# Kernel tuning notes

Hardware: AMD Instinct MI355X
Metric: run time of the kernel (lower is better)

Reference implementation:

```python
import jax, jax.numpy as jnp
import numpy as np

B, N, D, H = 128, 256, 256, 256
N_POWER_ITERS = 5  # matches spectral_norm(n_power_iterations=5)


def setup_inputs() -> dict:
    key = jax.random.key(0)
    ks = jax.random.split(key, 8)
    w = lambda k, shape: jax.random.normal(k, shape, dtype=jnp.float32) * 0.05
    return {
        "x": jax.random.normal(ks[0], (B, N, D), dtype=jnp.float32),
        "Wq": w(ks[1], (H, D)), "bq": w(ks[2], (H,)),
        "Wk": w(ks[3], (H, D)), "bk": w(ks[4], (H,)),
        "Wv": w(ks[5], (D, D)), "bv": w(ks[6], (D,)),
        "u0": jax.random.normal(ks[7], (D,), dtype=jnp.float32),
    }


def _l2norm(v, eps=1e-12):
    return v / (jnp.linalg.norm(v) + eps)


def _spectral_normalize(W, u0):
    # torch spectral_norm: power iteration (no grad) to get u, v; sigma = u^T W v (with grad)
    u = _l2norm(u0)
    v = _l2norm(W.T @ u)
    def body(i, uv):
        u, v = uv
        v = _l2norm(W.T @ u)
        u = _l2norm(W @ v)
        return (u, v)
    u, v = jax.lax.fori_loop(0, N_POWER_ITERS, body, (u, v))
    u = jax.lax.stop_gradient(u)
    v = jax.lax.stop_gradient(v)
    sigma = u @ (W @ v)
    return W / sigma


def reference(x, Wq, bq, Wk, bk, Wv, bv, u0):
    # torch Linear: y = x @ W.T + b, W is [out, in]
    q = jnp.einsum('bnd,hd->bnh', x, Wq) + bq          # [B, N, H]
    k = jnp.einsum('bnd,hd->bnh', x, Wk) + bk          # [B, N, H]
    Wv_sn = _spectral_normalize(Wv, u0)
    vals = jnp.einsum('bnd,od->bno', x, Wv_sn) + bv    # [B, N, D]
    scores = jnp.einsum('bnh,bmh->bnm', q, k)          # [B, N, N]
    # track_grads=False -> eigenvals detached; stop_gradient input so eig has no tangent path
    ev = jnp.linalg.eigvals(jax.lax.stop_gradient(scores))  # complex [B, N]
    rho = jnp.max(jnp.abs(ev), axis=-1)[:, None, None]      # spectral radius [B,1,1]
    attention = scores / rho
    weighted = jnp.einsum('bnm,bmd->bnd', attention, vals)  # [B, N, D]
    return weighted, attention
```

## Files before the change

kernel.cpp:

```cpp
#include <hip/hip_runtime.h>
#include <hip/hip_bf16.h>


#define NB 128
#define MAT 65536
#define BIG 8388608LL

typedef __attribute__((ext_vector_type(4))) float floatx4;
typedef __attribute__((ext_vector_type(4))) float f4v;
typedef __attribute__((ext_vector_type(8))) short short8v;
typedef __attribute__((ext_vector_type(4))) short short4v;

__device__ __forceinline__ short f2bf(float x) {
  union { float f; unsigned u; } v; v.f = x;
  unsigned r = v.u + 0x7fff + ((v.u >> 16) & 1);
  return (short)(r >> 16);
}
__device__ __forceinline__ float bf2f(short h) {
  union { unsigned u; float f; } v; v.u = ((unsigned)(unsigned short)h) << 16; return v.f;
}

template<bool TB, bool BATCHED>
__global__ __launch_bounds__(256) void gemm_mfma(
    const float* __restrict__ A, const float* __restrict__ B, float* __restrict__ C,
    long long sA, long long sB, long long sC,
    const float* __restrict__ bias,
    const float* __restrict__ scale_ptr, int sstride, int smode,
    float* __restrict__ norm_out,
    float* __restrict__ att_out,
    const float* __restrict__ B2, const float* __restrict__ bias2, float* __restrict__ C2,
    const float* __restrict__ B3, float* __restrict__ C3,
    const float* __restrict__ bsc, const float* __restrict__ bsb)
{
  __shared__ short sAhi[128 * 32], sAlo[128 * 32];
  __shared__ short sBhi[128 * 40], sBlo[128 * 40];

  int bz, m0, n0;
  if constexpr (BATCHED) {
    int lin = blockIdx.x;
    int xcd = lin & 7;
    int s = lin >> 3;
    bz = xcd * 16 + (s >> 2);
    int tile = s & 3;
    m0 = (tile >> 1) * 128;
    n0 = (tile & 1) * 128;
  } else {
    bz = 0;
    m0 = blockIdx.y * 128;
    n0 = (blockIdx.x & 1) * 128;
    int sel = blockIdx.x >> 1;
    if (sel == 1) { B = B2; bias = bias2; C = C2; }
    else if (sel == 2) { B = B3; bias = nullptr; C = C3; }
  }
  A += (long long)bz * sA;
  B += (long long)bz * sB;
  C += (long long)bz * sC;

  const int t = threadIdx.x;
  const int lane = t & 63;
  const int wave = t >> 6;
  const int wm = wave >> 1, wn = wave & 1;
  const int q = lane >> 4, c16 = lane & 15;

  float alpha = 1.0f;
  if (smode == 1) alpha = 1.0f / scale_ptr[bz * sstride];
  else if (smode == 2) alpha = scale_ptr[bz * sstride];

  float rinv_att = alpha;
  const bool do_att = (att_out != nullptr) && (n0 == 0);

  float binv = 1.0f;
  if (bsc) binv = 1.0f / bsc[0];

  floatx4 acc[4][4];
  #pragma unroll
  for (int i = 0; i < 4; i++)
    #pragma unroll
    for (int j = 0; j < 4; j++)
      acc[i][j] = (floatx4){0.f, 0.f, 0.f, 0.f};

  for (int k0 = 0; k0 < 256; k0 += 32) {
    #pragma unroll
    for (int i = 0; i < 4; i++) {
      int f = t + i * 256;
      int row = f >> 3, c4 = f & 7;
      f4v v = *(const f4v*)(A + (long long)(m0 + row) * 256 + k0 + c4 * 4);
      if (do_att)
        *(f4v*)(att_out + (long long)bz * MAT + (long long)(m0 + row) * 256 + k0 + c4 * 4)
            = v * rinv_att;
      short4v h, l;
      #pragma unroll
      for (int e = 0; e < 4; e++) {
        short hh = f2bf(v[e]);
        h[e] = hh;
        l[e] = f2bf(v[e] - bf2f(hh));
      }
      *(short4v*)&sAhi[row * 32 + c4 * 4] = h;
      *(short4v*)&sAlo[row * 32 + c4 * 4] = l;
    }
    if constexpr (TB) {
      #pragma unroll
      for (int i = 0; i < 4; i++) {
        int f = t + i * 256;
        int row = f >> 3, c4 = f & 7;
        f4v v = *(const f4v*)(B + (long long)(n0 + row) * 256 + k0 + c4 * 4);
        short4v h, l;
        #pragma unroll
        for (int e = 0; e < 4; e++) {
          short hh = f2bf(v[e]);
          h[e] = hh;
          l[e] = f2bf(v[e] - bf2f(hh));
        }
        *(short4v*)&sBhi[row * 40 + c4 * 4] = h;
        *(short4v*)&sBlo[row * 40 + c4 * 4] = l;
      }
      __syncthreads();
    } else {
      __shared__ float sT[32 * 132];
      #pragma unroll
      for (int i = 0; i < 4; i++) {
        int f = t + i * 256;
        int kk = f >> 5, n4 = f & 31;
        f4v v = *(const f4v*)(B + (long long)(k0 + kk) * 256 + n0 + n4 * 4);
        if (bsb) {
          #pragma unroll
          for (int e = 0; e < 4; e++) v[e] = v[e] * binv + bsb[n0 + n4 * 4 + e];
        }
        *(f4v*)&sT[kk * 132 + n4 * 4] = v;
      }
      __syncthreads();
      int n = t & 127, kh = t >> 7;
      short8v h0, h1, l0, l1;
      #pragma unroll
      for (int j = 0; j < 8; j++) {
        float x0 = sT[(kh * 16 + j) * 132 + n];
        float x1 = sT[(kh * 16 + 8 + j) * 132 + n];
        short a0 = f2bf(x0), a1 = f2bf(x1);
        h0[j] = a0; l0[j] = f2bf(x0 - bf2f(a0));
        h1[j] = a1; l1[j] = f2bf(x1 - bf2f(a1));
      }
      *(short8v*)&sBhi[n * 40 + kh * 16] = h0;
      *(short8v*)&sBhi[n * 40 + kh * 16 + 8] = h1;
      *(short8v*)&sBlo[n * 40 + kh * 16] = l0;
      *(short8v*)&sBlo[n * 40 + kh * 16 + 8] = l1;
      __syncthreads();
    }

    short8v ah[4], al[4], bh[4], bl[4];
    #pragma unroll
    for (int fi = 0; fi < 4; fi++) {
      int r = wm * 64 + fi * 16 + c16;
      ah[fi] = *(short8v*)&sAhi[r * 32 + q * 8];
      al[fi] = *(short8v*)&sAlo[r * 32 + q * 8];
    }
    #pragma unroll
    for (int fj = 0; fj < 4; fj++) {
      int r = wn * 64 + fj * 16 + c16;
      bh[fj] = *(short8v*)&sBhi[r * 40 + q * 8];
      bl[fj] = *(short8v*)&sBlo[r * 40 + q * 8];
    }
    #pragma unroll
    for (int fi = 0; fi < 4; fi++)
      #pragma unroll
      for (int fj = 0; fj < 4; fj++) {
        acc[fi][fj] = __builtin_amdgcn_mfma_f32_16x16x32_bf16(al[fi], bh[fj], acc[fi][fj], 0, 0, 0);
        acc[fi][fj] = __builtin_amdgcn_mfma_f32_16x16x32_bf16(ah[fi], bl[fj], acc[fi][fj], 0, 0, 0);
        acc[fi][fj] = __builtin_amdgcn_mfma_f32_16x16x32_bf16(ah[fi], bh[fj], acc[fi][fj], 0, 0, 0);
      }
    __syncthreads();
  }

  float ssq = 0.f;
  #pragma unroll
  for (int fi = 0; fi < 4; fi++) {
    #pragma unroll
    for (int fj = 0; fj < 4; fj++) {
      int col = n0 + wn * 64 + fj * 16 + c16;
      float bb = bias ? bias[col] : 0.f;
      #pragma unroll
      for (int r = 0; r < 4; r++) {
        int row = m0 + wm * 64 + fi * 16 + q * 4 + r;
        float v = acc[fi][fj][r] * alpha + bb;
        C[(long long)row * 256 + col] = v;
        ssq += v * v;
      }
    }
  }

  if (norm_out) {
    float* red = (float*)sAhi;
    red[t] = ssq;
    __syncthreads();
    for (int off = 128; off > 0; off >>= 1) {
      if (t < off) red[t] += red[t + off];
      __syncthreads();
    }
    if (t == 0) {
      int tl = ((m0 >> 7) << 1) | (n0 >> 7);
      norm_out[bz * 4 + tl] = red[0];
    }
  }
}

__global__ __launch_bounds__(256) void split_w(
    const float* __restrict__ Wq, const float* __restrict__ Wk,
    const float* __restrict__ Wv, short* __restrict__ ws6)
{
  int gid = blockIdx.x * 256 + threadIdx.x;
  int m = gid >> 14;
  int off = (gid & 16383) * 4;
  const float* src = (m == 0) ? Wq : (m == 1) ? Wk : Wv;
  f4v v = *(const f4v*)(src + off);
  short4v h, l;
  #pragma unroll
  for (int e = 0; e < 4; e++) {
    short hh = f2bf(v[e]);
    h[e] = hh;
    l[e] = f2bf(v[e] - bf2f(hh));
  }
  *(short4v*)&ws6[(long long)(m * 2) * MAT + off] = h;
  *(short4v*)&ws6[(long long)(m * 2 + 1) * MAT + off] = l;
}

__global__ __launch_bounds__(256) void proj_qkv(
    const float* __restrict__ x, const short* __restrict__ wsp,
    const float* __restrict__ bq, const float* __restrict__ bk,
    short* __restrict__ qhi, short* __restrict__ qlo,
    short* __restrict__ khi, short* __restrict__ klo,
    float* __restrict__ vals)
{
  __shared__ short sAhi[128 * 32], sAlo[128 * 32];
  __shared__ short sBhi[128 * 40], sBlo[128 * 40];

  const int lin = blockIdx.x;
  const int xcd = lin & 7;
  const int idx = lin >> 3;
  const int mloc = idx / 6;
  const int s6 = idx - mloc * 6;
  const int m0 = (xcd * 32 + mloc) * 128;
  const int sel = s6 >> 1;
  const int n0 = (s6 & 1) * 128;

  const short* wb_hi = wsp + (long long)(sel * 2) * MAT;
  const short* wb_lo = wsp + (long long)(sel * 2 + 1) * MAT;

  const int t = threadIdx.x;
  const int lane = t & 63;
  const int wave = t >> 6;
  const int wm = wave >> 1, wn = wave & 1;
  const int q = lane >> 4, c16 = lane & 15;

  floatx4 acc[4][4];
  #pragma unroll
  for (int i = 0; i < 4; i++)
    #pragma unroll
    for (int j = 0; j < 4; j++)
      acc[i][j] = (floatx4){0.f, 0.f, 0.f, 0.f};

  for (int k0 = 0; k0 < 256; k0 += 32) {
    #pragma unroll
    for (int i = 0; i < 4; i++) {
      int f = t + i * 256;
      int row = f >> 3, c4 = f & 7;
      f4v v = *(const f4v*)(x + (long long)(m0 + row) * 256 + k0 + c4 * 4);
      short4v h, l;
      #pragma unroll
      for (int e = 0; e < 4; e++) {
        short hh = f2bf(v[e]);
        h[e] = hh;
        l[e] = f2bf(v[e] - bf2f(hh));
      }
      *(short4v*)&sAhi[row * 32 + c4 * 4] = h;
      *(short4v*)&sAlo[row * 32 + c4 * 4] = l;
    }
    #pragma unroll
    for (int i = 0; i < 2; i++) {
      int chunk = t + i * 256;
      int row = chunk >> 2, c8 = chunk & 3;
      long long gr = (long long)(n0 + row) * 256 + k0 + c8 * 8;
      *(short8v*)&sBhi[row * 40 + c8 * 8] = *(const short8v*)(wb_hi + gr);
      *(short8v*)&sBlo[row * 40 + c8 * 8] = *(const short8v*)(wb_lo + gr);
    }
    __syncthreads();

    short8v ah[4], al[4], bh[4], bl[4];
    #pragma unroll
    for (int fi = 0; fi < 4; fi++) {
      int r = wm * 64 + fi * 16 + c16;
      ah[fi] = *(short8v*)&sAhi[r * 32 + q * 8];
      al[fi] = *(short8v*)&sAlo[r * 32 + q * 8];
    }
    #pragma unroll
    for (int fj = 0; fj < 4; fj++) {
      int r = wn * 64 + fj * 16 + c16;
      bh[fj] = *(short8v*)&sBhi[r * 40 + q * 8];
      bl[fj] = *(short8v*)&sBlo[r * 40 + q * 8];
    }
    #pragma unroll
    for (int fi = 0; fi < 4; fi++)
      #pragma unroll
      for (int fj = 0; fj < 4; fj++) {
        acc[fi][fj] = __builtin_amdgcn_mfma_f32_16x16x32_bf16(al[fi], bh[fj], acc[fi][fj], 0, 0, 0);
        acc[fi][fj] = __builtin_amdgcn_mfma_f32_16x16x32_bf16(ah[fi], bl[fj], acc[fi][fj], 0, 0, 0);
        acc[fi][fj] = __builtin_amdgcn_mfma_f32_16x16x32_bf16(ah[fi], bh[fj], acc[fi][fj], 0, 0, 0);
      }
    __syncthreads();
  }

  if (sel < 2) {
    short* ohi = sel ? khi : qhi;
    short* olo = sel ? klo : qlo;
    const float* bb = sel ? bk : bq;
    #pragma unroll
    for (int fi = 0; fi < 4; fi++)
      #pragma unroll
      for (int fj = 0; fj < 4; fj++) {
        int col = n0 + wn * 64 + fj * 16 + c16;
        float b = bb[col];
        #pragma unroll
        for (int r = 0; r < 4; r++) {
          long long row = m0 + wm * 64 + fi * 16 + q * 4 + r;
          float v = acc[fi][fj][r] + b;
          short h = f2bf(v);
          ohi[row * 256 + col] = h;
          olo[row * 256 + col] = f2bf(v - bf2f(h));
        }
      }
  } else {
    #pragma unroll
    for (int fi = 0; fi < 4; fi++)
      #pragma unroll
      for (int fj = 0; fj < 4; fj++) {
        int col = n0 + wn * 64 + fj * 16 + c16;
        #pragma unroll
        for (int r = 0; r < 4; r++) {
          long long row = m0 + wm * 64 + fi * 16 + q * 4 + r;
          vals[row * 256 + col] = acc[fi][fj][r];
        }
      }
  }
}

__global__ __launch_bounds__(256) void scores_st(
    const short* __restrict__ qhi, const short* __restrict__ qlo,
    const short* __restrict__ khi, const short* __restrict__ klo,
    float* __restrict__ S, float* __restrict__ norm_out)
{
  __shared__ short sAhi[128 * 32], sAlo[128 * 32];
  __shared__ short sBhi[128 * 40], sBlo[128 * 40];
  __shared__ float red[256];

  const int lin = blockIdx.x;
  const int xcd = lin & 7, s = lin >> 3;
  const int bz = xcd * 16 + (s >> 2);
  const int tile = s & 3;
  const int m0 = (tile >> 1) * 128, n0 = (tile & 1) * 128;

  const int t = threadIdx.x;
  const int lane = t & 63;
  const int wave = t >> 6;
  const int wm = wave >> 1, wn = wave & 1;
  const int q = lane >> 4, c16 = lane & 15;

  floatx4 acc[4][4];
  #pragma unroll
  for (int i = 0; i < 4; i++)
    #pragma unroll
    for (int j = 0; j < 4; j++)
      acc[i][j] = (floatx4){0.f, 0.f, 0.f, 0.f};

  const long long abase = (long long)(bz * 256 + m0) * 256;
  const long long bbase = (long long)(bz * 256 + n0) * 256;

  for (int k0 = 0; k0 < 256; k0 += 32) {
    #pragma unroll
    for (int i = 0; i < 2; i++) {
      int chunk = t + i * 256;
      int row = chunk >> 2, c8 = chunk & 3;
      long long ga = abase + (long long)row * 256 + k0 + c8 * 8;
      long long gb = bbase + (long long)row * 256 + k0 + c8 * 8;
      *(short8v*)&sAhi[row * 32 + c8 * 8] = *(const short8v*)(qhi + ga);
      *(short8v*)&sAlo[row * 32 + c8 * 8] = *(const short8v*)(qlo + ga);
      *(short8v*)&sBhi[row * 40 + c8 * 8] = *(const short8v*)(khi + gb);
      *(short8v*)&sBlo[row * 40 + c8 * 8] = *(const short8v*)(klo + gb);
    }
    __syncthreads();

    short8v ah[4], al[4], bh[4], bl[4];
    #pragma unroll
    for (int fi = 0; fi < 4; fi++) {
      int r = wm * 64 + fi * 16 + c16;
      ah[fi] = *(short8v*)&sAhi[r * 32 + q * 8];
      al[fi] = *(short8v*)&sAlo[r * 32 + q * 8];
    }
    #pragma unroll
    for (int fj = 0; fj < 4; fj++) {
      int r = wn * 64 + fj * 16 + c16;
      bh[fj] = *(short8v*)&sBhi[r * 40 + q * 8];
      bl[fj] = *(short8v*)&sBlo[r * 40 + q * 8];
    }
    #pragma unroll
    for (int fi = 0; fi < 4; fi++)
      #pragma unroll
      for (int fj = 0; fj < 4; fj++) {
        acc[fi][fj] = __builtin_amdgcn_mfma_f32_16x16x32_bf16(al[fi], bh[fj], acc[fi][fj], 0, 0, 0);
        acc[fi][fj] = __builtin_amdgcn_mfma_f32_16x16x32_bf16(ah[fi], bl[fj], acc[fi][fj], 0, 0, 0);
        acc[fi][fj] = __builtin_amdgcn_mfma_f32_16x16x32_bf16(ah[fi], bh[fj], acc[fi][fj], 0, 0, 0);
      }
    __syncthreads();
  }

  float* C = S + (long long)bz * MAT;
  float ssq = 0.f;
  #pragma unroll
  for (int fi = 0; fi < 4; fi++)
    #pragma unroll
    for (int fj = 0; fj < 4; fj++) {
      int col = n0 + wn * 64 + fj * 16 + c16;
      #pragma unroll
      for (int r = 0; r < 4; r++) {
        int row = m0 + wm * 64 + fi * 16 + q * 4 + r;
        float v = acc[fi][fj][r];
        C[(long long)row * 256 + col] = v;
        ssq += v * v;
      }
    }

  red[t] = ssq;
  __syncthreads();
  for (int off = 128; off > 0; off >>= 1) {
    if (t < off) red[t] += red[t + off];
    __syncthreads();
  }
  if (t == 0) norm_out[bz * 4 + tile] = red[0];
}

__device__ __forceinline__ void chain_epilogue(
    short* LB, float* red, floatx4 (&acc)[4][4], float alpha,
    int m0, int n0, int wm, int wn, int q, int c16, int t,
    short* __restrict__ Mout,
    float* __restrict__ nout, int bz, int tile, bool write_out)
{
  __syncthreads();
  float ssq = 0.f;
  #pragma unroll
  for (int fi = 0; fi < 4; fi++)
    #pragma unroll
    for (int fj = 0; fj < 4; fj++) {
      int lcol = wn * 64 + fj * 16 + c16;
      #pragma unroll
      for (int r = 0; r < 4; r++) {
        int lrow = wm * 64 + fi * 16 + q * 4 + r;
        float v = acc[fi][fj][r] * alpha;
        ssq += v * v;
        if (write_out) LB[lrow * 128 + lcol] = f2bf(v);
      }
    }

  if (write_out) {
    __syncthreads();
    int lr = t >> 1, off = (t & 1) * 64;
    #pragma unroll
    for (int jc = 0; jc < 8; jc++)
      *(short8v*)(Mout + (long long)(m0 + lr) * 256 + n0 + off + jc * 8)
          = *(const short8v*)&LB[lr * 128 + off + jc * 8];
  }

  red[t] = ssq;
  __syncthreads();
  for (int off2 = 128; off2 > 0; off2 >>= 1) {
    if (t < off2) red[t] += red[t + off2];
    __syncthreads();
  }
  if (t == 0) nout[bz * 4 + tile] = red[0];
}

__global__ __launch_bounds__(256) void sq_f32bf(
    const float* __restrict__ S, short* __restrict__ Mo,
    const float* __restrict__ nprev, float* __restrict__ nout)
{
  __shared__ short SM[18432];
  __shared__ float sT[32 * 132];
  __shared__ float red[256];
  short* sAhi = SM;
  short* sAlo = SM + 4096;
  short* sBhi = SM + 8192;
  short* sBlo = SM + 13312;

  int lin = blockIdx.x;
  int xcd = lin & 7, s = lin >> 3;
  int bz = xcd * 16 + (s >> 2);
  int tile = s & 3;
  int m0 = (tile >> 1) * 128, n0 = (tile & 1) * 128;
  const float* A = S + (long long)bz * MAT;

  const int t = threadIdx.x;
  const int lane = t & 63;
  const int wave = t >> 6;
  const int wm = wave >> 1, wn = wave & 1;
  const int q = lane >> 4, c16 = lane & 15;

  floatx4 acc[4][4];
  #pragma unroll
  for (int i = 0; i < 4; i++)
    #pragma unroll
    for (int j = 0; j < 4; j++)
      acc[i][j] = (floatx4){0.f, 0.f, 0.f, 0.f};

  for (int k0 = 0; k0 < 256; k0 += 32) {
    #pragma unroll
    for (int i = 0; i < 4; i++) {
      int f = t + i * 256;
      int row = f >> 3, c4 = f & 7;
      f4v v = *(const f4v*)(A + (long long)(m0 + row) * 256 + k0 + c4 * 4);
      short4v h, l;
      #pragma unroll
      for (int e = 0; e < 4; e++) {
        short hh = f2bf(v[e]);
        h[e] = hh;
        l[e] = f2bf(v[e] - bf2f(hh));
      }
      *(short4v*)&sAhi[row * 32 + c4 * 4] = h;
      *(short4v*)&sAlo[row * 32 + c4 * 4] = l;
    }
    #pragma unroll
    for (int i = 0; i < 4; i++) {
      int f = t + i * 256;
      int kk = f >> 5, n4 = f & 31;
      f4v v = *(const f4v*)(A + (long long)(k0 + kk) * 256 + n0 + n4 * 4);
      *(f4v*)&sT[kk * 132 + n4 * 4] = v;
    }
    __syncthreads();
    {
      int n = t & 127, kh = t >> 7;
      short8v h0, h1, l0, l1;
      #pragma unroll
      for (int j = 0; j < 8; j++) {
        float x0 = sT[(kh * 16 + j) * 132 + n];
        float x1 = sT[(kh * 16 + 8 + j) * 132 + n];
        short a0 = f2bf(x0), a1 = f2bf(x1);
        h0[j] = a0; l0[j] = f2bf(x0 - bf2f(a0));
        h1[j] = a1; l1[j] = f2bf(x1 - bf2f(a1));
      }
      *(short8v*)&sBhi[n * 40 + kh * 16] = h0;
      *(short8v*)&sBhi[n * 40 + kh * 16 + 8] = h1;
      *(short8v*)&sBlo[n * 40 + kh * 16] = l0;
      *(short8v*)&sBlo[n * 40 + kh * 16 + 8] = l1;
    }
    __syncthreads();

    short8v ah[4], al[4], bh[4], bl[4];
    #pragma unroll
    for (int fi = 0; fi < 4; fi++) {
      int r = wm * 64 + fi * 16 + c16;
      ah[fi] = *(short8v*)&sAhi[r * 32 + q * 8];
      al[fi] = *(short8v*)&sAlo[r * 32 + q * 8];
    }
    #pragma unroll
    for (int fj = 0; fj < 4; fj++) {
      int r = wn * 64 + fj * 16 + c16;
      bh[fj] = *(short8v*)&sBhi[r * 40 + q * 8];
      bl[fj] = *(short8v*)&sBlo[r * 40 + q * 8];
    }
    #pragma unroll
    for (int fi = 0; fi < 4; fi++)
      #pragma unroll
      for (int fj = 0; fj < 4; fj++) {
        acc[fi][fj] = __builtin_amdgcn_mfma_f32_16x16x32_bf16(al[fi], bh[fj], acc[fi][fj], 0, 0, 0);
        acc[fi][fj] = __builtin_amdgcn_mfma_f32_16x16x32_bf16(ah[fi], bl[fj], acc[fi][fj], 0, 0, 0);
        acc[fi][fj] = __builtin_amdgcn_mfma_f32_16x16x32_bf16(ah[fi], bh[fj], acc[fi][fj], 0, 0, 0);
      }
    __syncthreads();
  }

  const float* p = nprev + bz * 4;
  float alpha = 1.0f / (p[0] + p[1] + p[2] + p[3]);
  chain_epilogue(SM, red, acc, alpha, m0, n0, wm, wn, q, c16, t,
                 Mo + (long long)bz * MAT, nout, bz, tile, true);
}

template<bool WRITE_OUT>
__global__ __launch_bounds__(256) void sq_bf(
    const short* __restrict__ Mi, short* __restrict__ Mo,
    const float* __restrict__ nprev, float* __restrict__ nout)
{
  __shared__ short SMEM[16384];
  __shared__ float red[256];
  short* Bs = SMEM;

  int lin = blockIdx.x;
  int xcd = lin & 7, s = lin >> 3;
  int bz = xcd * 16 + (s >> 2);
  int tile = s & 3;
  int m0 = (tile >> 1) * 128, n0 = (tile & 1) * 128;

  const short* A = Mi + (long long)bz * MAT;

  const int t = threadIdx.x;
  const int lane = t & 63;
  const int wave = t >> 6;
  const int wm = wave >> 1, wn = wave & 1;
  const int q = lane >> 4, c16 = lane & 15;
  const int g = t >> 5, cc = t & 31;

  floatx4 acc[4][4];
  #pragma unroll
  for (int i = 0; i < 4; i++)
    #pragma unroll
    for (int j = 0; j < 4; j++)
      acc[i][j] = (floatx4){0.f, 0.f, 0.f, 0.f};

  short4v r0 = *(const short4v*)(A + (long long)(g * 4 + 0) * 256 + n0 + cc * 4);
  short4v r1 = *(const short4v*)(A + (long long)(g * 4 + 1) * 256 + n0 + cc * 4);
  short4v r2 = *(const short4v*)(A + (long long)(g * 4 + 2) * 256 + n0 + cc * 4);
  short4v r3 = *(const short4v*)(A + (long long)(g * 4 + 3) * 256 + n0 + cc * 4);

  for (int k0 = 0; k0 < 256; k0 += 32) {
    __syncthreads();
    #pragma unroll
    for (int j = 0; j < 4; j++) {
      short4v w4 = (short4v){r0[j], r1[j], r2[j], r3[j]};
      *(short4v*)&Bs[(cc * 4 + j) * 36 + g * 4] = w4;
    }
    __syncthreads();

    if (k0 < 224) {
      int kn = k0 + 32;
      r0 = *(const short4v*)(A + (long long)(kn + g * 4 + 0) * 256 + n0 + cc * 4);
      r1 = *(const short4v*)(A + (long long)(kn + g * 4 + 1) * 256 + n0 + cc * 4);
      r2 = *(const short4v*)(A + (long long)(kn + g * 4 + 2) * 256 + n0 + cc * 4);
      r3 = *(const short4v*)(A + (long long)(kn + g * 4 + 3) * 256 + n0 + cc * 4);
    }

    short8v a[4], b[4];
    #pragma unroll
    for (int fi = 0; fi < 4; fi++)
      a[fi] = *(const short8v*)(A + (long long)(m0 + wm * 64 + fi * 16 + c16) * 256 + k0 + q * 8);
    #pragma unroll
    for (int fj = 0; fj < 4; fj++) {
      int n = wn * 64 + fj * 16 + c16;
      short4v lo = *(const short4v*)&Bs[n * 36 + q * 8];
      short4v hi = *(const short4v*)&Bs[n * 36 + q * 8 + 4];
      b[fj] = __builtin_shufflevector(lo, hi, 0, 1, 2, 3, 4, 5, 6, 7);
    }
    #pragma unroll
    for (int fi = 0; fi < 4; fi++)
      #pragma unroll
      for (int fj = 0; fj < 4; fj++)
        acc[fi][fj] = __builtin_amdgcn_mfma_f32_16x16x32_bf16(a[fi], b[fj], acc[fi][fj], 0, 0, 0);
  }

  const float* p = nprev + bz * 4;
  float alpha = 1.0f / (p[0] + p[1] + p[2] + p[3]);
  chain_epilogue(SMEM, red, acc, alpha, m0, n0, wm, wn, q, c16, t,
                 WRITE_OUT ? Mo + (long long)bz * MAT : nullptr,
                 nout, bz, tile, WRITE_OUT);
}

__global__ __launch_bounds__(128) void rho_finalize(
    const float* __restrict__ partials, float* __restrict__ rho_inv)
{
  int bz = threadIdx.x;
  float a2 = 0.f, w = 1.0f;
  #pragma unroll
  for (int i2 = 0; i2 <= 12; i2++) {
    const float* p = partials + i2 * 512 + bz * 4;
    a2 += w * 0.5f * logf(p[0] + p[1] + p[2] + p[3]);
    w *= 0.5f;
  }
  rho_inv[bz] = expf(-a2);
}

__device__ __forceinline__ float bsum1024(float x, float* red, int t)
{
  red[t] = x; __syncthreads();
  for (int off = 512; off > 0; off >>= 1) {
    if (t < off) red[t] += red[t + off];
    __syncthreads();
  }
  float r = red[0];
  __syncthreads();
  return r;
}

__global__ __launch_bounds__(1024) void sigma_kernel(
    const float* __restrict__ W, const float* __restrict__ u0, float* __restrict__ sigma)
{
  __shared__ short Wl[65536];
  __shared__ float u[256], v[256], red[1024];
  int t = threadIdx.x;
  int r = t & 255, seg = t >> 8;
  const float eps = 1e-12f;

  #pragma unroll
  for (int i = 0; i < 16; i++) {
    int idx = (i * 1024 + t) * 4;
    f4v w = *(const f4v*)(W + idx);
    short4v h;
    #pragma unroll
    for (int e = 0; e < 4; e++) h[e] = f2bf(w[e]);
    *(short4v*)&Wl[idx] = h;
  }

  float x = (t < 256) ? u0[t] : 0.f;
  float nrm = sqrtf(bsum1024(x * x, red, t));
  if (t < 256) u[t] = x / (nrm + eps);
  __syncthreads();

  for (int it = 0; it < 5; it++) {
    float sv = 0.f;
    #pragma unroll 8
    for (int j = 0; j < 64; j++) {
      int h = seg * 64 + j;
      sv = fmaf(bf2f(Wl[h * 256 + r]), u[h], sv);
    }
    red[t] = sv; __syncthreads();
    float vr = 0.f;
    if (t < 256) vr = red[t] + red[256 + t] + red[512 + t] + red[768 + t];
    __syncthreads();
    nrm = sqrtf(bsum1024(t < 256 ? vr * vr : 0.f, red, t));
    if (t < 256) v[t] = vr / (nrm + eps);
    __syncthreads();
    if (it < 4) {
      float su = 0.f;
      #pragma unroll
      for (int j = 0; j < 16; j++) {
        short4v w4 = *(const short4v*)&Wl[r * 256 + seg * 64 + j * 4];
        const float* vv = &v[seg * 64 + j * 4];
        su += bf2f(w4[0]) * vv[0] + bf2f(w4[1]) * vv[1]
            + bf2f(w4[2]) * vv[2] + bf2f(w4[3]) * vv[3];
      }
      red[t] = su; __syncthreads();
      float ur = 0.f;
      if (t < 256) ur = red[t] + red[256 + t] + red[512 + t] + red[768 + t];
      __syncthreads();
      nrm = sqrtf(bsum1024(t < 256 ? ur * ur : 0.f, red, t));
      if (t < 256) u[t] = ur / (nrm + eps);
      __syncthreads();
    }
  }

  float z = 0.f;
  #pragma unroll
  for (int j = 0; j < 16; j++) {
    f4v w = *(const f4v*)(W + r * 256 + seg * 64 + j * 4);
    const float* vv = &v[seg * 64 + j * 4];
    z += w[0] * vv[0] + w[1] * vv[1] + w[2] * vv[2] + w[3] * vv[3];
  }
  red[t] = z; __syncthreads();
  float zr = 0.f;
  if (t < 256) zr = red[t] + red[256 + t] + red[512 + t] + red[768 + t];
  __syncthreads();
  float zz = bsum1024(t < 256 ? zr * zr : 0.f, red, t);
  if (t == 0) sigma[0] = sqrtf(zz);
}

extern "C" void kernel_launch(void* const* d_in, const int* in_sizes, int n_in,
                              void* d_out, int out_size, void* d_ws, size_t ws_size,
                              hipStream_t stream)
{
  const float* x  = (const float*)d_in[0];
  const float* Wq = (const float*)d_in[1];
  const float* bq = (const float*)d_in[2];
  const float* Wk = (const float*)d_in[3];
  const float* bk = (const float*)d_in[4];
  const float* Wv = (const float*)d_in[5];
  const float* bv = (const float*)d_in[6];
  const float* u0 = (const float*)d_in[7];

  float* out  = (float*)d_out;
  float* out0 = out;
  float* out1 = out + BIG;
  short* out0s = (short*)out0;
  short* out1s = (short*)out1;

  short* qhi = out0s;
  short* qlo = out0s + 32768LL * 256;
  short* khi = out1s;
  short* klo = out1s + 32768LL * 256;

  float* ws         = (float*)d_ws;
  float* scores_buf = ws;
  float* vals_buf   = ws + BIG;
  float* partials   = ws + 2 * BIG;
  float* sigma      = partials + 13 * 512;
  float* rho_inv    = sigma + 4;
  short* wsplit     = (short*)ws;

  dim3 blk(256);

  split_w<<<dim3(192, 1, 1), blk, 0, stream>>>(Wq, Wk, Wv, wsplit);

  proj_qkv<<<dim3(1536, 1, 1), blk, 0, stream>>>(
      x, wsplit, bq, bk, qhi, qlo, khi, klo, vals_buf);

  scores_st<<<dim3(512, 1, 1), blk, 0, stream>>>(
      qhi, qlo, khi, klo, scores_buf, partials);

  sigma_kernel<<<1, dim3(1024), 0, stream>>>(Wv, u0, sigma);

  sq_f32bf<<<dim3(512, 1, 1), blk, 0, stream>>>(scores_buf, out0s, partials, partials + 512);

  const short* cin = out0s;
  for (int i = 0; i < 10; i++) {
    short* cout = (i & 1) ? out0s : out1s;
    sq_bf<true><<<dim3(512, 1, 1), blk, 0, stream>>>(cin, cout,
        partials + (1 + i) * 512, partials + (2 + i) * 512);
    cin = cout;
  }
  sq_bf<false><<<dim3(512, 1, 1), blk, 0, stream>>>(cin, nullptr,
      partials + 11 * 512, partials + 12 * 512);

  rho_finalize<<<1, dim3(128), 0, stream>>>(partials, rho_inv);

  gemm_mfma<false, true><<<dim3(512, 1, 1), blk, 0, stream>>>(
      scores_buf, vals_buf, out0, MAT, MAT, MAT, nullptr, rho_inv, 1, 2, nullptr,
      out1, nullptr, nullptr, nullptr, nullptr, nullptr, sigma, bv);
}
```

Baseline: 484.2 us.

## Pre-split x into bf16 hi/lo once and double-buffer sq_bf LDS staging

x is converted to bf16 hi/lo pairs once in a widened split kernel, so proj_qkv no longer re-converts each x tile for every one of the six output tiles that read it. proj_qkv now loads the pre-split values with plain vector loads. Separately, sq_bf alternates between two LDS buffers for the transposed B tile, which removes one __syncthreads per k-step. The cost is an extra round trip of x through the workspace (write hi/lo, read back) and a relocated weight-split buffer.

```diff
diff --git a/kernel.cpp b/kernel.cpp
--- a/kernel.cpp
+++ b/kernel.cpp
@@ -202,28 +202,49 @@
   }
 }
 
-__global__ __launch_bounds__(256) void split_w(
+__global__ __launch_bounds__(256) void split_inputs(
     const float* __restrict__ Wq, const float* __restrict__ Wk,
-    const float* __restrict__ Wv, short* __restrict__ ws6)
-{
-  int gid = blockIdx.x * 256 + threadIdx.x;
-  int m = gid >> 14;
-  int off = (gid & 16383) * 4;
-  const float* src = (m == 0) ? Wq : (m == 1) ? Wk : Wv;
-  f4v v = *(const f4v*)(src + off);
-  short4v h, l;
-  #pragma unroll
-  for (int e = 0; e < 4; e++) {
-    short hh = f2bf(v[e]);
-    h[e] = hh;
-    l[e] = f2bf(v[e] - bf2f(hh));
-  }
-  *(short4v*)&ws6[(long long)(m * 2) * MAT + off] = h;
-  *(short4v*)&ws6[(long long)(m * 2 + 1) * MAT + off] = l;
+    const float* __restrict__ Wv, short* __restrict__ ws6,
+    const float* __restrict__ x, short* __restrict__ xhi, short* __restrict__ xlo)
+{
+  int b = blockIdx.x;
+  int t = threadIdx.x;
+  if (b < 192) {
+    int gid = b * 256 + t;
+    int m = gid >> 14;
+    int off = (gid & 16383) * 4;
+    const float* src = (m == 0) ? Wq : (m == 1) ? Wk : Wv;
+    f4v v = *(const f4v*)(src + off);
+    short4v h, l;
+    #pragma unroll
+    for (int e = 0; e < 4; e++) {
+      short hh = f2bf(v[e]);
+      h[e] = hh;
+      l[e] = f2bf(v[e] - bf2f(hh));
+    }
+    *(short4v*)&ws6[(long long)(m * 2) * MAT + off] = h;
+    *(short4v*)&ws6[(long long)(m * 2 + 1) * MAT + off] = l;
+  } else {
+    long long off = ((long long)(b - 192) * 256 + t) * 8;
+    #pragma unroll
+    for (int half = 0; half < 2; half++) {
+      f4v v = *(const f4v*)(x + off + half * 4);
+      short4v h, l;
+      #pragma unroll
+      for (int e = 0; e < 4; e++) {
+        short hh = f2bf(v[e]);
+        h[e] = hh;
+        l[e] = f2bf(v[e] - bf2f(hh));
+      }
+      *(short4v*)&xhi[off + half * 4] = h;
+      *(short4v*)&xlo[off + half * 4] = l;
+    }
+  }
 }
 
 __global__ __launch_bounds__(256) void proj_qkv(
-    const float* __restrict__ x, const short* __restrict__ wsp,
+    const short* __restrict__ xhi, const short* __restrict__ xlo,
+    const short* __restrict__ wsp,
     const float* __restrict__ bq, const float* __restrict__ bk,
     short* __restrict__ qhi, short* __restrict__ qlo,
     short* __restrict__ khi, short* __restrict__ klo,
@@ -259,19 +280,12 @@
 
   for (int k0 = 0; k0 < 256; k0 += 32) {
     #pragma unroll
-    for (int i = 0; i < 4; i++) {
-      int f = t + i * 256;
-      int row = f >> 3, c4 = f & 7;
-      f4v v = *(const f4v*)(x + (long long)(m0 + row) * 256 + k0 + c4 * 4);
-      short4v h, l;
-      #pragma unroll
-      for (int e = 0; e < 4; e++) {
-        short hh = f2bf(v[e]);
-        h[e] = hh;
-        l[e] = f2bf(v[e] - bf2f(hh));
-      }
-      *(short4v*)&sAhi[row * 32 + c4 * 4] = h;
-      *(short4v*)&sAlo[row * 32 + c4 * 4] = l;
+    for (int i = 0; i < 2; i++) {
+      int chunk = t + i * 256;
+      int row = chunk >> 2, c8 = chunk & 3;
+      long long ga = (long long)(m0 + row) * 256 + k0 + c8 * 8;
+      *(short8v*)&sAhi[row * 32 + c8 * 8] = *(const short8v*)(xhi + ga);
+      *(short8v*)&sAlo[row * 32 + c8 * 8] = *(const short8v*)(xlo + ga);
     }
     #pragma unroll
     for (int i = 0; i < 2; i++) {
@@ -586,7 +600,8 @@
 {
   __shared__ short SMEM[16384];
   __shared__ float red[256];
-  short* Bs = SMEM;
+  short* BsA = SMEM;
+  short* BsB = SMEM + 4608;
 
   int lin = blockIdx.x;
   int xcd = lin & 7, s = lin >> 3;
@@ -616,11 +631,11 @@
   short4v r3 = *(const short4v*)(A + (long long)(g * 4 + 3) * 256 + n0 + cc * 4);
 
   for (int k0 = 0; k0 < 256; k0 += 32) {
-    __syncthreads();
+    short* Bw = ((k0 >> 5) & 1) ? BsB : BsA;
     #pragma unroll
     for (int j = 0; j < 4; j++) {
       short4v w4 = (short4v){r0[j], r1[j], r2[j], r3[j]};
-      *(short4v*)&Bs[(cc * 4 + j) * 36 + g * 4] = w4;
+      *(short4v*)&Bw[(cc * 4 + j) * 36 + g * 4] = w4;
     }
     __syncthreads();
 
@@ -639,8 +654,8 @@
     #pragma unroll
     for (int fj = 0; fj < 4; fj++) {
       int n = wn * 64 + fj * 16 + c16;
-      short4v lo = *(const short4v*)&Bs[n * 36 + q * 8];
-      short4v hi = *(const short4v*)&Bs[n * 36 + q * 8 + 4];
+      short4v lo = *(const short4v*)&Bw[n * 36 + q * 8];
+      short4v hi = *(const short4v*)&Bw[n * 36 + q * 8 + 4];
       b[fj] = __builtin_shufflevector(lo, hi, 0, 1, 2, 3, 4, 5, 6, 7);
     }
     #pragma unroll
@@ -785,14 +800,17 @@
   float* partials   = ws + 2 * BIG;
   float* sigma      = partials + 13 * 512;
   float* rho_inv    = sigma + 4;
-  short* wsplit     = (short*)ws;
+  short* wsplit     = (short*)(rho_inv + 128);
+
+  short* xhi = (short*)scores_buf;
+  short* xlo = xhi + BIG;
 
   dim3 blk(256);
 
-  split_w<<<dim3(192, 1, 1), blk, 0, stream>>>(Wq, Wk, Wv, wsplit);
+  split_inputs<<<dim3(4288, 1, 1), blk, 0, stream>>>(Wq, Wk, Wv, wsplit, x, xhi, xlo);
 
   proj_qkv<<<dim3(1536, 1, 1), blk, 0, stream>>>(
-      x, wsplit, bq, bk, qhi, qlo, khi, klo, vals_buf);
+      xhi, xlo, wsplit, bq, bk, qhi, qlo, khi, klo, vals_buf);
 
   scores_st<<<dim3(512, 1, 1), blk, 0, stream>>>(
       qhi, qlo, khi, klo, scores_buf, partials);
```

New measurement: 479.3 us. About the same (-1.0%).
